# Kernel tuning notes

Hardware: AMD Instinct MI355X
Metric: run time of the kernel (lower is better)

Reference implementation:

```python
import jax, jax.numpy as jnp
import numpy as np

EPSILON = 1e-05
B, H, P, T, D = 256, 8, 64, 3, 64

def setup_inputs() -> dict:
    key = jax.random.key(0)
    ks = jax.random.split(key, 7)
    return {
        "X": jax.random.normal(ks[0], (B, H, P, T), dtype=jnp.float32),
        "W_left": jax.random.normal(ks[1], (H, P, D), dtype=jnp.float32),
        "W_right": jax.random.normal(ks[2], (H, P, D), dtype=jnp.float32),
        "fc1_w": jax.random.normal(ks[3], (D, H * P * D), dtype=jnp.float32) / np.sqrt(H * P * D),
        "fc1_b": jax.random.normal(ks[4], (D,), dtype=jnp.float32) * 0.01,
        "fc2_w": jax.random.normal(ks[5], (1, D), dtype=jnp.float32) / np.sqrt(D),
        "fc2_b": jax.random.normal(ks[6], (1,), dtype=jnp.float32) * 0.01,
    }

def reference(X, W_left, W_right, fc1_w, fc1_b, fc2_w, fc2_b):
    # pairwise deltas: [B,h,i,j,t]
    delta = X[..., :, None, :] - X[..., None, :, :]
    # relu(delta^2) is a no-op mathematically but kept faithful
    distance = jnp.sqrt(jnp.maximum(delta * delta, 0.0) + EPSILON)
    dX = (delta / distance) * jnp.exp(-distance)  # direction * exp(-dist)
    Xl = jnp.einsum('nhijt,hjd->nhidt', dX, W_left)
    Xr = jnp.einsum('nhijt,hjd->nhidt', dX, W_right)
    att = jnp.einsum('nhidt,nhidt->nhid', Xl, Xr)  # reduce over t
    flat = att.reshape(att.shape[0], -1)  # [B, h*p*d]
    hdn = jax.nn.silu(flat @ fc1_w.T + fc1_b)
    return hdn @ fc2_w.T + fc2_b  # [B, 1]
```

## Files before the change

kernel.cpp:

```cpp
#include <hip/hip_runtime.h>
#include <hip/hip_bf16.h>


typedef __attribute__((ext_vector_type(8))) short short8;
typedef __attribute__((ext_vector_type(4))) float f32x4;

#define PADW 72
#define PADM 2056
#define KTOT 32768L

__device__ __forceinline__ unsigned short f2b(float x) {
  union { float f; unsigned int u; } v; v.f = x;
  return (unsigned short)((v.u + 0x7FFFu + ((v.u >> 16) & 1u)) >> 16);
}

__device__ __forceinline__ unsigned int pk_bf16(float a, float b) {
  unsigned int r;
  asm("v_cvt_pk_bf16_f32 %0, %1, %2" : "=v"(r) : "v"(a), "v"(b));
  return r;
}

__global__ __launch_bounds__(512, 1)
void k_fused(const float* __restrict__ X, const float* __restrict__ Wl_g,
             const float* __restrict__ Wr_g,
             const float* __restrict__ fc1w,
             float* __restrict__ partial) {
  __shared__ float xs[16][3][64];
  __shared__ __align__(16) union {
    struct {
      unsigned short wl[64][PADW];
      unsigned short wr[64][PADW];
      unsigned short dxs[2][3][32][PADW];
    } a;
    float red[8][16][64];
  } u;
  __shared__ __align__(16) unsigned short att_s[16][PADM];

  const int blk  = blockIdx.x;
  const int ih   = blk & 1;
  const int h    = (blk >> 1) & 7;
  const int ng   = blk >> 4;
  const int tid  = threadIdx.x;
  const int lane = tid & 63;
  const int w    = tid >> 6;
  const int c0   = lane & 15;
  const int ks   = lane >> 4;
  const int iw   = (w >> 1) & 1;
  const int dw   = w & 1;
  const int qsub = w >> 2;

  const float* wlg = Wl_g + h * 4096;
  const float* wrg = Wr_g + h * 4096;
#pragma unroll
  for (int r = 0; r < 8; ++r) {
    int e = tid + r * 512;
    int j = e >> 6, d = e & 63;
    u.a.wl[d][j] = f2b(wlg[e]);
    u.a.wr[d][j] = f2b(wrg[e]);
  }
  {
    const long xbase = ((long)(ng * 16) * 8 + h) * 192;
#pragma unroll
    for (int r = 0; r < 6; ++r) {
      int e = tid + r * 512;
      int q = e / 192;
      int rem = e - q * 192;
      int i = rem / 3;
      int t = rem - i * 3;
      xs[q][t][i] = X[xbase + (long)q * 1536 + rem];
    }
  }
  __syncthreads();

  short8 bl[2][2], br[2][2];
#pragma unroll
  for (int cb = 0; cb < 2; ++cb)
#pragma unroll
    for (int kb = 0; kb < 2; ++kb) {
      const int d = c0 + 16 * cb + 32 * dw;
      const int j0 = ks * 8 + 32 * kb;
      bl[cb][kb] = *(const short8*)&u.a.wl[d][j0];
      br[cb][kb] = *(const short8*)&u.a.wr[d][j0];
    }

  const int dq  = tid >> 8;
  const int il  = (tid >> 3) & 31;
  const int jb  = (tid & 7) << 3;

  for (int it = 0; it < 8; ++it) {
    const int qd = it * 2 + dq;
    if (it) __syncthreads();
#pragma unroll
    for (int t = 0; t < 3; ++t) {
      const float xi = xs[qd][t][ih * 32 + il];
#pragma unroll
      for (int jj = 0; jj < 8; jj += 2) {
        float d0 = xi - xs[qd][t][jb + jj];
        float d1 = xi - xs[qd][t][jb + jj + 1];
        float s0 = d0 * d0 + 1e-5f;
        float s1 = d1 * d1 + 1e-5f;
        float i0 = __builtin_amdgcn_rsqf(s0);
        float i1 = __builtin_amdgcn_rsqf(s1);
        float e0 = __builtin_amdgcn_exp2f(-1.44269504f * (s0 * i0));
        float e1 = __builtin_amdgcn_exp2f(-1.44269504f * (s1 * i1));
        *(unsigned int*)&u.a.dxs[dq][t][il][jb + jj] =
            pk_bf16(d0 * i0 * e0, d1 * i1 * e1);
      }
    }
    __syncthreads();

    const int q = it * 2 + qsub;
    f32x4 acc[2];
#pragma unroll
    for (int cb = 0; cb < 2; ++cb) {
      acc[cb][0] = 0.f; acc[cb][1] = 0.f; acc[cb][2] = 0.f; acc[cb][3] = 0.f;
    }
#pragma unroll
    for (int t = 0; t < 3; ++t) {
      short8 a0 = *(const short8*)&u.a.dxs[qsub][t][iw * 16 + c0][ks * 8];
      short8 a1 = *(const short8*)&u.a.dxs[qsub][t][iw * 16 + c0][ks * 8 + 32];
#pragma unroll
      for (int cb = 0; cb < 2; ++cb) {
        f32x4 xl; xl[0]=0.f; xl[1]=0.f; xl[2]=0.f; xl[3]=0.f;
        f32x4 xr; xr[0]=0.f; xr[1]=0.f; xr[2]=0.f; xr[3]=0.f;
        xl = __builtin_amdgcn_mfma_f32_16x16x32_bf16(a0, bl[cb][0], xl, 0, 0, 0);
        xl = __builtin_amdgcn_mfma_f32_16x16x32_bf16(a1, bl[cb][1], xl, 0, 0, 0);
        xr = __builtin_amdgcn_mfma_f32_16x16x32_bf16(a0, br[cb][0], xr, 0, 0, 0);
        xr = __builtin_amdgcn_mfma_f32_16x16x32_bf16(a1, br[cb][1], xr, 0, 0, 0);
        acc[cb] += xl * xr;
      }
    }
#pragma unroll
    for (int cb = 0; cb < 2; ++cb)
#pragma unroll
      for (int r = 0; r < 4; ++r) {
        int ro = iw * 16 + ks * 4 + r;
        int d = c0 + 16 * cb + 32 * dw;
        att_s[q][ro * 64 + d] = f2b(acc[cb][r]);
      }
  }
  __syncthreads();

  f32x4 facc[4];
#pragma unroll
  for (int cb = 0; cb < 4; ++cb) {
    facc[cb][0] = 0.f; facc[cb][1] = 0.f; facc[cb][2] = 0.f; facc[cb][3] = 0.f;
  }
  const float* bpf =
      fc1w + (long)c0 * KTOT + h * 4096 + ih * 2048 + w * 256 + ks * 8;
  const unsigned short* ap = &att_s[0][0] + c0 * PADM + w * 256 + ks * 8;
#pragma unroll
  for (int s = 0; s < 8; ++s) {
    short8 a = *(const short8*)(ap + s * 32);
#pragma unroll
    for (int cb = 0; cb < 4; ++cb) {
      const float* src = bpf + (long)cb * 16 * KTOT + s * 32;
      f32x4 v0 = *(const f32x4*)(src);
      f32x4 v1 = *(const f32x4*)(src + 4);
      union { unsigned short us[8]; short8 s8; } pw;
      pw.us[0] = f2b(v0[0]);
      pw.us[1] = f2b(v0[1]);
      pw.us[2] = f2b(v0[2]);
      pw.us[3] = f2b(v0[3]);
      pw.us[4] = f2b(v1[0]);
      pw.us[5] = f2b(v1[1]);
      pw.us[6] = f2b(v1[2]);
      pw.us[7] = f2b(v1[3]);
      facc[cb] = __builtin_amdgcn_mfma_f32_16x16x32_bf16(a, pw.s8, facc[cb], 0, 0, 0);
    }
  }
  __syncthreads();
#pragma unroll
  for (int cb = 0; cb < 4; ++cb)
#pragma unroll
    for (int r = 0; r < 4; ++r)
      u.red[w][ks * 4 + r][c0 + 16 * cb] = facc[cb][r];
  __syncthreads();
#pragma unroll
  for (int rep = 0; rep < 2; ++rep) {
    int e = tid + rep * 512;
    int nl = e >> 6, k = e & 63;
    float s = 0.f;
#pragma unroll
    for (int ww = 0; ww < 8; ++ww) s += u.red[ww][nl][k];
    partial[(((long)h * 2 + ih) * 256 + ng * 16 + nl) * 64 + k] = s;
  }
}

__global__ __launch_bounds__(256)
void k_fc2(const float* __restrict__ partial, const float* __restrict__ fc1_b,
           const float* __restrict__ fc2_w, const float* __restrict__ fc2_b,
           float* __restrict__ out) {
  const int tid = threadIdx.x;
  const int n = blockIdx.x * 4 + (tid >> 6);
  const int k = tid & 63;
  float s = fc1_b[k];
#pragma unroll
  for (int sp = 0; sp < 16; ++sp)
    s += partial[((long)sp * 256 + n) * 64 + k];
  float g = s / (1.f + __expf(-s));
  float v = g * fc2_w[k];
#pragma unroll
  for (int off = 32; off > 0; off >>= 1)
    v += __shfl_xor(v, off, 64);
  if (k == 0) out[n] = v + fc2_b[0];
}

extern "C" void kernel_launch(void* const* d_in, const int* in_sizes, int n_in,
                              void* d_out, int out_size, void* d_ws, size_t ws_size,
                              hipStream_t stream) {
  const float* X    = (const float*)d_in[0];
  const float* Wl   = (const float*)d_in[1];
  const float* Wr   = (const float*)d_in[2];
  const float* fc1w = (const float*)d_in[3];
  const float* fc1b = (const float*)d_in[4];
  const float* fc2w = (const float*)d_in[5];
  const float* fc2b = (const float*)d_in[6];
  float* out = (float*)d_out;

  float* partial = (float*)d_ws;

  hipLaunchKernelGGL(k_fused, dim3(256), dim3(512), 0, stream, X, Wl, Wr, fc1w, partial);
  hipLaunchKernelGGL(k_fc2,   dim3(64), dim3(256), 0, stream, partial, fc1b, fc2w, fc2b, out);
}
```

Baseline: 38.52 us.

## Split i dimension into four quarters per block to double grid size

The fused kernel now assigns each block 16 rows of i (four quarters) instead of 32, doubling the grid from 256 to 512 blocks and halving the shared att buffer and dxs tile. Warp roles are remapped so each warp computes one 16-wide d block for one batch sub-slice, and launch bounds now request up to 4 blocks per CU. The aim is to fill more CUs and improve occupancy, at the cost of recomputing the W loads per block and producing twice as many fc1 partial sums for the second kernel to reduce.

```diff
diff --git a/kernel.cpp b/kernel.cpp
--- a/kernel.cpp
+++ b/kernel.cpp
@@ -6,7 +6,7 @@
 typedef __attribute__((ext_vector_type(4))) float f32x4;
 
 #define PADW 72
-#define PADM 2056
+#define PADM 1032
 #define KTOT 32768L
 
 __device__ __forceinline__ unsigned short f2b(float x) {
@@ -20,7 +20,7 @@
   return r;
 }
 
-__global__ __launch_bounds__(512, 1)
+__global__ __launch_bounds__(512, 4)
 void k_fused(const float* __restrict__ X, const float* __restrict__ Wl_g,
              const float* __restrict__ Wr_g,
              const float* __restrict__ fc1w,
@@ -30,24 +30,23 @@
     struct {
       unsigned short wl[64][PADW];
       unsigned short wr[64][PADW];
-      unsigned short dxs[2][3][32][PADW];
+      unsigned short dxs[2][3][16][PADW];
     } a;
     float red[8][16][64];
   } u;
   __shared__ __align__(16) unsigned short att_s[16][PADM];
 
   const int blk  = blockIdx.x;
-  const int ih   = blk & 1;
-  const int h    = (blk >> 1) & 7;
-  const int ng   = blk >> 4;
+  const int iq   = blk & 3;
+  const int h    = (blk >> 2) & 7;
+  const int ng   = blk >> 5;
   const int tid  = threadIdx.x;
   const int lane = tid & 63;
   const int w    = tid >> 6;
   const int c0   = lane & 15;
   const int ks   = lane >> 4;
-  const int iw   = (w >> 1) & 1;
-  const int dw   = w & 1;
-  const int qsub = w >> 2;
+  const int qsub = w & 1;
+  const int dblk = w >> 1;
 
   const float* wlg = Wl_g + h * 4096;
   const float* wrg = Wr_g + h * 4096;
@@ -72,72 +71,62 @@
   }
   __syncthreads();
 
-  short8 bl[2][2], br[2][2];
-#pragma unroll
-  for (int cb = 0; cb < 2; ++cb)
-#pragma unroll
-    for (int kb = 0; kb < 2; ++kb) {
-      const int d = c0 + 16 * cb + 32 * dw;
-      const int j0 = ks * 8 + 32 * kb;
-      bl[cb][kb] = *(const short8*)&u.a.wl[d][j0];
-      br[cb][kb] = *(const short8*)&u.a.wr[d][j0];
-    }
-
-  const int dq  = tid >> 8;
-  const int il  = (tid >> 3) & 31;
-  const int jb  = (tid & 7) << 3;
+  short8 bl[2], br[2];
+#pragma unroll
+  for (int kb = 0; kb < 2; ++kb) {
+    const int d = dblk * 16 + c0;
+    const int j0 = ks * 8 + 32 * kb;
+    bl[kb] = *(const short8*)&u.a.wl[d][j0];
+    br[kb] = *(const short8*)&u.a.wr[d][j0];
+  }
+
+  const int dq = tid >> 8;
+  const int il = (tid >> 4) & 15;
+  const int j4 = (tid & 15) << 2;
 
   for (int it = 0; it < 8; ++it) {
     const int qd = it * 2 + dq;
     if (it) __syncthreads();
 #pragma unroll
     for (int t = 0; t < 3; ++t) {
-      const float xi = xs[qd][t][ih * 32 + il];
-#pragma unroll
-      for (int jj = 0; jj < 8; jj += 2) {
-        float d0 = xi - xs[qd][t][jb + jj];
-        float d1 = xi - xs[qd][t][jb + jj + 1];
-        float s0 = d0 * d0 + 1e-5f;
-        float s1 = d1 * d1 + 1e-5f;
-        float i0 = __builtin_amdgcn_rsqf(s0);
-        float i1 = __builtin_amdgcn_rsqf(s1);
-        float e0 = __builtin_amdgcn_exp2f(-1.44269504f * (s0 * i0));
-        float e1 = __builtin_amdgcn_exp2f(-1.44269504f * (s1 * i1));
-        *(unsigned int*)&u.a.dxs[dq][t][il][jb + jj] =
-            pk_bf16(d0 * i0 * e0, d1 * i1 * e1);
-      }
+      const float xi = xs[qd][t][iq * 16 + il];
+      float d0 = xi - xs[qd][t][j4];
+      float d1 = xi - xs[qd][t][j4 + 1];
+      float d2 = xi - xs[qd][t][j4 + 2];
+      float d3 = xi - xs[qd][t][j4 + 3];
+      float s0 = d0 * d0 + 1e-5f, s1 = d1 * d1 + 1e-5f;
+      float s2 = d2 * d2 + 1e-5f, s3 = d3 * d3 + 1e-5f;
+      float i0 = __builtin_amdgcn_rsqf(s0), i1 = __builtin_amdgcn_rsqf(s1);
+      float i2 = __builtin_amdgcn_rsqf(s2), i3 = __builtin_amdgcn_rsqf(s3);
+      float e0 = __builtin_amdgcn_exp2f(-1.44269504f * (s0 * i0));
+      float e1 = __builtin_amdgcn_exp2f(-1.44269504f * (s1 * i1));
+      float e2 = __builtin_amdgcn_exp2f(-1.44269504f * (s2 * i2));
+      float e3 = __builtin_amdgcn_exp2f(-1.44269504f * (s3 * i3));
+      *(unsigned int*)&u.a.dxs[dq][t][il][j4] =
+          pk_bf16(d0 * i0 * e0, d1 * i1 * e1);
+      *(unsigned int*)&u.a.dxs[dq][t][il][j4 + 2] =
+          pk_bf16(d2 * i2 * e2, d3 * i3 * e3);
     }
     __syncthreads();
 
     const int q = it * 2 + qsub;
-    f32x4 acc[2];
-#pragma unroll
-    for (int cb = 0; cb < 2; ++cb) {
-      acc[cb][0] = 0.f; acc[cb][1] = 0.f; acc[cb][2] = 0.f; acc[cb][3] = 0.f;
-    }
+    f32x4 acc;
+    acc[0] = 0.f; acc[1] = 0.f; acc[2] = 0.f; acc[3] = 0.f;
 #pragma unroll
     for (int t = 0; t < 3; ++t) {
-      short8 a0 = *(const short8*)&u.a.dxs[qsub][t][iw * 16 + c0][ks * 8];
-      short8 a1 = *(const short8*)&u.a.dxs[qsub][t][iw * 16 + c0][ks * 8 + 32];
-#pragma unroll
-      for (int cb = 0; cb < 2; ++cb) {
-        f32x4 xl; xl[0]=0.f; xl[1]=0.f; xl[2]=0.f; xl[3]=0.f;
-        f32x4 xr; xr[0]=0.f; xr[1]=0.f; xr[2]=0.f; xr[3]=0.f;
-        xl = __builtin_amdgcn_mfma_f32_16x16x32_bf16(a0, bl[cb][0], xl, 0, 0, 0);
-        xl = __builtin_amdgcn_mfma_f32_16x16x32_bf16(a1, bl[cb][1], xl, 0, 0, 0);
-        xr = __builtin_amdgcn_mfma_f32_16x16x32_bf16(a0, br[cb][0], xr, 0, 0, 0);
-        xr = __builtin_amdgcn_mfma_f32_16x16x32_bf16(a1, br[cb][1], xr, 0, 0, 0);
-        acc[cb] += xl * xr;
-      }
-    }
-#pragma unroll
-    for (int cb = 0; cb < 2; ++cb)
-#pragma unroll
-      for (int r = 0; r < 4; ++r) {
-        int ro = iw * 16 + ks * 4 + r;
-        int d = c0 + 16 * cb + 32 * dw;
-        att_s[q][ro * 64 + d] = f2b(acc[cb][r]);
-      }
+      short8 a0 = *(const short8*)&u.a.dxs[qsub][t][c0][ks * 8];
+      short8 a1 = *(const short8*)&u.a.dxs[qsub][t][c0][ks * 8 + 32];
+      f32x4 xl; xl[0]=0.f; xl[1]=0.f; xl[2]=0.f; xl[3]=0.f;
+      f32x4 xr; xr[0]=0.f; xr[1]=0.f; xr[2]=0.f; xr[3]=0.f;
+      xl = __builtin_amdgcn_mfma_f32_16x16x32_bf16(a0, bl[0], xl, 0, 0, 0);
+      xl = __builtin_amdgcn_mfma_f32_16x16x32_bf16(a1, bl[1], xl, 0, 0, 0);
+      xr = __builtin_amdgcn_mfma_f32_16x16x32_bf16(a0, br[0], xr, 0, 0, 0);
+      xr = __builtin_amdgcn_mfma_f32_16x16x32_bf16(a1, br[1], xr, 0, 0, 0);
+      acc += xl * xr;
+    }
+#pragma unroll
+    for (int r = 0; r < 4; ++r)
+      att_s[q][(ks * 4 + r) * 64 + dblk * 16 + c0] = f2b(acc[r]);
   }
   __syncthreads();
 
@@ -147,10 +136,10 @@
     facc[cb][0] = 0.f; facc[cb][1] = 0.f; facc[cb][2] = 0.f; facc[cb][3] = 0.f;
   }
   const float* bpf =
-      fc1w + (long)c0 * KTOT + h * 4096 + ih * 2048 + w * 256 + ks * 8;
-  const unsigned short* ap = &att_s[0][0] + c0 * PADM + w * 256 + ks * 8;
-#pragma unroll
-  for (int s = 0; s < 8; ++s) {
+      fc1w + (long)c0 * KTOT + h * 4096 + iq * 1024 + w * 128 + ks * 8;
+  const unsigned short* ap = &att_s[0][0] + c0 * PADM + w * 128 + ks * 8;
+#pragma unroll
+  for (int s = 0; s < 4; ++s) {
     short8 a = *(const short8*)(ap + s * 32);
 #pragma unroll
     for (int cb = 0; cb < 4; ++cb) {
@@ -183,7 +172,7 @@
     float s = 0.f;
 #pragma unroll
     for (int ww = 0; ww < 8; ++ww) s += u.red[ww][nl][k];
-    partial[(((long)h * 2 + ih) * 256 + ng * 16 + nl) * 64 + k] = s;
+    partial[(((long)h * 4 + iq) * 256 + ng * 16 + nl) * 64 + k] = s;
   }
 }
 
@@ -196,7 +185,7 @@
   const int k = tid & 63;
   float s = fc1_b[k];
 #pragma unroll
-  for (int sp = 0; sp < 16; ++sp)
+  for (int sp = 0; sp < 32; ++sp)
     s += partial[((long)sp * 256 + n) * 64 + k];
   float g = s / (1.f + __expf(-s));
   float v = g * fc2_w[k];
@@ -220,6 +209,6 @@
 
   float* partial = (float*)d_ws;
 
-  hipLaunchKernelGGL(k_fused, dim3(256), dim3(512), 0, stream, X, Wl, Wr, fc1w, partial);
+  hipLaunchKernelGGL(k_fused, dim3(512), dim3(512), 0, stream, X, Wl, Wr, fc1w, partial);
   hipLaunchKernelGGL(k_fc2,   dim3(64), dim3(256), 0, stream, partial, fc1b, fc2w, fc2b, out);
 }
```

New measurement: 32.78 us. -14.9%, faster.
